# Optimization experiments

Measured on AMD Instinct MI355X. Metric: run time of the kernel, lower is better.

## Reference

```python
import jax, jax.numpy as jnp
import numpy as np

B, S, E, H, ROT, MAXP = 2, 1024, 2048, 16, 64, 2048
HD = E // H
EPS = 1e-12  # torch F.normalize default eps


def _sinusoidal_positions(num_pos, dim):
    # GPT-J create_sinusoidal_positions: concat(sin, cos) along feature dim
    inv_freq = 1.0 / (10000.0 ** (np.arange(0, dim, 2, dtype=np.float32) / dim))
    sinusoid = np.einsum("i,j->ij", np.arange(num_pos, dtype=np.float32), inv_freq)
    return jnp.asarray(np.concatenate([np.sin(sinusoid), np.cos(sinusoid)], axis=-1))


def _rotate_every_two(x):
    x1 = x[..., ::2]
    x2 = x[..., 1::2]
    return jnp.stack((-x2, x1), axis=-1).reshape(x.shape)


def _apply_rotary(t, sin, cos):
    # t: [B,S,H,rot]; sin/cos: [B,S,rot/2] -> repeat_interleave(2) -> [B,S,1,rot]
    sin = jnp.repeat(sin, 2, axis=-1)[:, :, None, :]
    cos = jnp.repeat(cos, 2, axis=-1)[:, :, None, :]
    return t * cos + _rotate_every_two(t) * sin


def setup_inputs() -> dict:
    key = jax.random.key(0)
    ks = jax.random.split(key, 5)
    hidden_states = jax.random.normal(ks[0], (B, S, E), dtype=jnp.float32)
    w_q = jax.random.normal(ks[1], (E, E), dtype=jnp.float32) * 0.02
    w_k = jax.random.normal(ks[2], (E, E), dtype=jnp.float32) * 0.02
    w_v = jax.random.normal(ks[3], (E, E), dtype=jnp.float32) * 0.02
    w_o = jax.random.normal(ks[4], (E, E), dtype=jnp.float32) * 0.02
    norm_const = 0.5 * jnp.ones((1, H, 1, 1), dtype=jnp.float32)
    attention_mask = jnp.zeros((B, 1, 1, S), dtype=jnp.float32)  # 0 = attend (HF additive mask)
    position_ids = jnp.tile(jnp.arange(S, dtype=jnp.int32)[None, :], (B, 1))
    return {"hidden_states": hidden_states, "w_q": w_q, "w_k": w_k, "w_v": w_v,
            "w_o": w_o, "norm_const": norm_const, "attention_mask": attention_mask,
            "position_ids": position_ids}


def reference(hidden_states, w_q, w_k, w_v, w_o, norm_const, attention_mask, position_ids):
    b, s, e = hidden_states.shape
    # projections (nn.Linear, no bias): y = x @ W.T
    q = (hidden_states @ w_q.T).reshape(b, s, H, HD)  # rotary layout [B,S,H,hd]
    k = (hidden_states @ w_k.T).reshape(b, s, H, HD)
    v = (hidden_states @ w_v.T).reshape(b, s, H, HD).transpose(0, 2, 1, 3)  # [B,H,S,hd]

    embed = _sinusoidal_positions(MAXP, ROT)          # [MAXP, ROT]
    sincos = embed[position_ids]                      # [B,S,ROT]
    sin, cos = jnp.split(sincos, 2, axis=-1)          # each [B,S,ROT/2]

    # partial rotary on first ROT dims
    q = jnp.concatenate([_apply_rotary(q[..., :ROT], sin, cos), q[..., ROT:]], axis=-1)
    k = jnp.concatenate([_apply_rotary(k[..., :ROT], sin, cos), k[..., ROT:]], axis=-1)
    q = q.transpose(0, 2, 1, 3)  # [B,H,S,hd]
    k = k.transpose(0, 2, 1, 3)

    causal = jnp.tril(jnp.ones((s, s), dtype=bool))[None, None]   # [1,1,S,S]
    mask0 = (attention_mask == 0)                                  # [B,1,1,S] bool

    # value rescale: per-query count of visible keys ** sigmoid(norm_const), clamped >= 1
    counts = jnp.sum(causal & mask0, axis=-1, keepdims=True).astype(jnp.float32)  # [B,1,S,1]
    denom = jnp.maximum(counts ** jax.nn.sigmoid(norm_const), 1.0)                # [B,H,S,1]
    v = v / denom

    # L2-normalize q/k (torch F.normalize: x / max(||x||, eps))
    q = q / jnp.maximum(jnp.linalg.norm(q, axis=-1, keepdims=True), EPS)
    k = k / jnp.maximum(jnp.linalg.norm(k, axis=-1, keepdims=True), EPS)

    mask_t = jnp.swapaxes(mask0, -1, -2)  # [B,1,S,1]
    q = q * mask_t
    k = k * mask_t
    v = v * mask_t

    attn_weights = jnp.einsum("bhqd,bhkd->bhqk", q, k)     # cosine similarities
    attn_weights = jnp.where(causal, attn_weights, 0.0)
    attn_output = jnp.einsum("bhqk,bhkd->bhqd", attn_weights, v)

    attn_output = attn_output.transpose(0, 2, 1, 3).reshape(b, s, e)
    return attn_output @ w_o.T
```

## Files before the change

kernel.cpp:

```cpp
#include <hip/hip_runtime.h>
#include <math.h>

#define B 2
#define S 1024
#define E 2048
#define H 16
#define HD 128
#define ROT 64
#define EPSN 1e-12f

using half8 = __attribute__((ext_vector_type(8))) _Float16;
using half4 = __attribute__((ext_vector_type(4))) _Float16;
using half2 = __attribute__((ext_vector_type(2))) _Float16;
using f32x4 = __attribute__((ext_vector_type(4))) float;

__device__ __forceinline__ void gl_lds16(const void* g, void* l) {
    __builtin_amdgcn_global_load_lds(
        (const __attribute__((address_space(1))) unsigned int*)g,
        (__attribute__((address_space(3))) unsigned int*)l, 16, 0, 0);
}

#define BARX()  asm volatile("s_barrier" ::: "memory")
#define LGKM0() asm volatile("s_waitcnt lgkmcnt(0)" ::: "memory")
#define VMW(n)  asm volatile("s_waitcnt vmcnt(" #n ")" ::: "memory")

__device__ __forceinline__ int ctIdx(int row, int col) {
    int f = (row & 15) ^ ((row >> 3) & 15);
    return row * 256 + (col & 3) + (((col >> 2) ^ f) << 2);
}

__global__ __launch_bounds__(256) void f2h5(const float* __restrict__ x0,
                                            const float* __restrict__ x1,
                                            const float* __restrict__ x2,
                                            const float* __restrict__ x3,
                                            const float* __restrict__ x4,
                                            _Float16* __restrict__ y0,
                                            _Float16* __restrict__ y1,
                                            _Float16* __restrict__ y2,
                                            _Float16* __restrict__ y3,
                                            _Float16* __restrict__ y4) {
    const float* xs[5] = {x0, x1, x2, x3, x4};
    _Float16*    ys[5] = {y0, y1, y2, y3, y4};
    const int t = blockIdx.y;
    const int i = blockIdx.x * 256 + threadIdx.x;
    float4 v = ((const float4*)xs[t])[i];
    half4 h;
    h[0] = (_Float16)v.x; h[1] = (_Float16)v.y;
    h[2] = (_Float16)v.z; h[3] = (_Float16)v.w;
    ((half4*)ys[t])[i] = h;
}

__global__ __launch_bounds__(1024) void countprep(const float* __restrict__ am,
                                                  const int* __restrict__ pos,
                                                  float* __restrict__ cnt,
                                                  float* __restrict__ tab) {
    __shared__ float sc[1024];
    const int b = blockIdx.x, t = threadIdx.x;
    sc[t] = (am[b * S + t] == 0.f) ? 1.f : 0.f;
    __syncthreads();
    for (int off = 1; off < 1024; off <<= 1) {
        float u = (t >= off) ? sc[t - off] : 0.f;
        __syncthreads();
        sc[t] += u;
        __syncthreads();
    }
    cnt[b * S + t] = sc[t];

    const float p = (float)pos[b * S + t];
    float* tp = &tab[((size_t)b * S + t) * 64];
#pragma unroll
    for (int j = 0; j < 32; ++j) {
        float ang = p * expf(-0.28782313662425574f * (float)j);
        float s_, c_;
        sincosf(ang, &s_, &c_);
        tp[j * 2]     = c_;
        tp[j * 2 + 1] = s_;
    }
}

__global__ __launch_bounds__(512, 2) void gemm_qkv256(
        const _Float16* __restrict__ hs,
        const _Float16* __restrict__ wq,
        const _Float16* __restrict__ wk,
        const _Float16* __restrict__ wv,
        _Float16* __restrict__ qo,
        _Float16* __restrict__ ko,
        _Float16* __restrict__ kto,
        _Float16* __restrict__ vto,
        const float* __restrict__ am,
        const float* __restrict__ nc,
        const float* __restrict__ cnt,
        const float* __restrict__ tab) {
    __shared__ uint4 L[8][1024];
    __shared__ float sclA[256], sclB[256];

    const int lid = (int)blockIdx.x;
    const int swz = (lid & 7) * 24 + (lid >> 3);
    const int z   = swz >> 6;
    const int gm  = (swz & 63) >> 3;
    const int gn  = swz & 7;
    const _Float16* Wp = (z == 0) ? wq : (z == 1) ? wk : wv;
    const int mBase = gm << 8;
    const int nBase = gn << 8;

    const int tid   = (int)threadIdx.x;
    const int lane  = tid & 63;
    const int w     = tid >> 6;
    const int l15   = lane & 15;
    const int lq    = lane >> 4;
    const int wm4   = (w >> 2) << 2;
    const int wn2   = (w & 3) << 1;
    const int wbase = tid & 448;

    const int bb  = mBase >> 10;
    const int sB0 = mBase & (S - 1);
    const int h0  = gn * 2;

    if (tid < 256) {
        const int sgx = sB0 + tid;
        float valid = (am[bb * S + sgx] == 0.f) ? 1.f : 0.f;
        if (z == 2) {
            float c  = cnt[bb * S + sgx];
            float g0 = 1.f / (1.f + expf(-nc[h0]));
            float g1 = 1.f / (1.f + expf(-nc[h0 + 1]));
            sclA[tid] = valid / fmaxf(powf(c, g0), 1.f);
            sclB[tid] = valid / fmaxf(powf(c, g1), 1.f);
        } else {
            sclA[tid] = valid;
        }
    }

    f32x4 acc[2][2][4][2];
#pragma unroll
    for (int X = 0; X < 2; ++X)
#pragma unroll
        for (int Y = 0; Y < 2; ++Y)
#pragma unroll
            for (int mt = 0; mt < 4; ++mt)
#pragma unroll
                for (int nt = 0; nt < 2; ++nt)
                    acc[X][Y][mt][nt] = (f32x4){0.f, 0.f, 0.f, 0.f};

    half8 af[4][2], wf[2][2];

    auto stage = [&](int slot, const _Float16* src, int rowBase, int hf, int kt) {
#pragma unroll
        for (int j = 0; j < 2; ++j) {
            const int c  = (j << 9) + tid;
            const int rb = c >> 7;
            const int q  = (c >> 4) & 7;
            const int r  = c & 15;
            gl_lds16(&src[(size_t)(rowBase + hf * 128 + rb * 16 + r) * E +
                          kt * 64 + q * 8],
                     &L[slot][(j << 9) + wbase]);
        }
    };
    auto ldsA = [&](int db, int X) {
#pragma unroll
        for (int mt = 0; mt < 4; ++mt)
#pragma unroll
            for (int ks = 0; ks < 2; ++ks)
                af[mt][ks] = *(const half8*)&L[db * 2 + X]
                    [(wm4 + mt) * 128 + (ks * 4 + lq) * 16 + l15];
    };
    auto ldsB = [&](int db, int Y) {
#pragma unroll
        for (int nt = 0; nt < 2; ++nt)
#pragma unroll
            for (int ks = 0; ks < 2; ++ks)
                wf[nt][ks] = *(const half8*)&L[4 + db * 2 + Y]
                    [(wn2 + nt) * 128 + (ks * 4 + lq) * 16 + l15];
    };
    auto mma = [&](int X, int Y) {
        __builtin_amdgcn_s_setprio(1);
#pragma unroll
        for (int mt = 0; mt < 4; ++mt)
#pragma unroll
            for (int nt = 0; nt < 2; ++nt)
#pragma unroll
                for (int ks = 0; ks < 2; ++ks)
                    acc[X][Y][mt][nt] = __builtin_amdgcn_mfma_f32_16x16x32_f16(
                        af[mt][ks], wf[nt][ks], acc[X][Y][mt][nt], 0, 0, 0);
        __builtin_amdgcn_s_setprio(0);
    };

    stage(0, hs, mBase, 0, 0);
    stage(4, Wp, nBase, 0, 0);
    stage(1, hs, mBase, 1, 0);
    stage(5, Wp, nBase, 1, 0);
    stage(2, hs, mBase, 0, 1);
    stage(7, Wp, nBase, 1, 1);
    stage(3, hs, mBase, 1, 1);
    VMW(6);
    BARX();

    for (int j = 0; j < 16; ++j) {
        const int tB  = 2 * j + 1;
        const int tN0 = 2 * j + 2;
        const int tN1 = 2 * j + 3;
        const bool more = (j < 15);

        ldsA(0, 0); ldsB(0, 0);
        stage(6, Wp, nBase, 0, tB);
        BARX(); LGKM0();
        mma(0, 0);
        BARX();

        ldsB(0, 1);
        if (more) stage(0, hs, mBase, 0, tN0);
        BARX(); LGKM0();
        mma(0, 1);
        BARX();

        ldsA(0, 1);
        if (more) stage(5, Wp, nBase, 1, tN0);
        BARX(); LGKM0();
        mma(1, 1);
        BARX();

        ldsB(0, 0);
        if (more) { stage(1, hs, mBase, 1, tN0); VMW(4); }
        else      { VMW(0); }
        BARX(); LGKM0();
        mma(1, 0);
        BARX();

        ldsA(1, 0); ldsB(1, 0);
        if (more) stage(4, Wp, nBase, 0, tN0);
        BARX(); LGKM0();
        mma(0, 0);
        BARX();

        ldsB(1, 1);
        if (more) stage(2, hs, mBase, 0, tN1);
        BARX(); LGKM0();
        mma(0, 1);
        BARX();

        ldsA(1, 1);
        if (more) stage(7, Wp, nBase, 1, tN1);
        BARX(); LGKM0();
        mma(1, 1);
        BARX();

        ldsB(1, 0);
        if (more) stage(3, hs, mBase, 1, tN1);
        VMW(4);
        BARX(); LGKM0();
        mma(1, 0);
        BARX();
    }

    VMW(0);
    BARX();
    _Float16* CtH = (_Float16*)&L[0][0];
#pragma unroll
    for (int X = 0; X < 2; ++X)
#pragma unroll
        for (int Y = 0; Y < 2; ++Y)
#pragma unroll
            for (int mt = 0; mt < 4; ++mt)
#pragma unroll
                for (int nt = 0; nt < 2; ++nt)
#pragma unroll
                    for (int r = 0; r < 4; ++r) {
                        int row = X * 128 + (w >> 2) * 64 + mt * 16 + lq * 4 + r;
                        int col = Y * 128 + (w & 3) * 32 + nt * 16 + l15;
                        float v = acc[X][Y][mt][nt][r];
                        if (z == 2) v *= (Y ? sclB[row] : sclA[row]);
                        CtH[ctIdx(row, col)] = (_Float16)v;
                    }
    __syncthreads();

    if (z < 2) {
        const int row = tid >> 1;
        const int hh  = tid & 1;
        const int sg  = sB0 + row;
        const float* tb = &tab[((size_t)bb * S + sg) * 64];

        half4 gv[32];
        float ss = 0.f;
#pragma unroll
        for (int k = 0; k < 32; ++k) {
            half4 x = *(const half4*)&CtH[ctIdx(row, hh * 128 + k * 4)];
            float v0 = x[0], v1 = x[1], v2 = x[2], v3 = x[3];
            if (k < 16) {
                float4 t4 = *(const float4*)&tb[k * 4];
                float t0 = v0 * t4.x - v1 * t4.y;
                float t1 = v1 * t4.x + v0 * t4.y;
                float t2 = v2 * t4.z - v3 * t4.w;
                float t3 = v3 * t4.z + v2 * t4.w;
                v0 = t0; v1 = t1; v2 = t2; v3 = t3;
            }
            ss += v0 * v0 + v1 * v1 + v2 * v2 + v3 * v3;
            half4 y;
            y[0] = (_Float16)v0; y[1] = (_Float16)v1;
            y[2] = (_Float16)v2; y[3] = (_Float16)v3;
            gv[k] = y;
        }
        float scl = sclA[row] / fmaxf(sqrtf(ss), EPSN);
        _Float16* rowOut = (z == 0) ? qo : ko;
        _Float16* gp = &rowOut[(((size_t)bb * H + h0 + hh) * S + sg) * HD];
#pragma unroll
        for (int k = 0; k < 32; ++k) {
            half4 y;
            y[0] = (_Float16)((float)gv[k][0] * scl);
            y[1] = (_Float16)((float)gv[k][1] * scl);
            y[2] = (_Float16)((float)gv[k][2] * scl);
            y[3] = (_Float16)((float)gv[k][3] * scl);
            *(half4*)&gp[k * 4] = y;
            if (z == 1)
                *(half4*)&CtH[ctIdx(row, hh * 128 + k * 4)] = y;
        }
    }
    if (z >= 1) {
        if (z == 1) __syncthreads();
        _Float16* To = (z == 1) ? kto : vto;
#pragma unroll
        for (int i = 0; i < 16; ++i) {
            int cch = tid + i * 512;
            int dr  = cch >> 5;
            int sc  = cch & 31;
            half8 hv;
#pragma unroll
            for (int jj = 0; jj < 8; ++jj)
                hv[jj] = CtH[ctIdx(sc * 8 + jj, dr)];
            *(half8*)&To[(((size_t)bb * H + h0 + (dr >> 7)) * HD + (dr & 127)) * S +
                         sB0 + sc * 8] = hv;
        }
    }
}

__global__ __launch_bounds__(256) void gemm_out(const _Float16* __restrict__ A,
                                                const _Float16* __restrict__ Wp,
                                                float* __restrict__ C) {
    __shared__ uint4 As_l[2][512];
    __shared__ uint4 Ws_l[2][512];
    const int lid = (int)blockIdx.x;
    const int swz = (lid & 7) * 32 + (lid >> 3);
    const int gm  = swz >> 4;
    const int gn  = swz & 15;
    const int tid  = threadIdx.x;
    const int lane = tid & 63;
    const int w    = tid >> 6;
    const int wm   = (w >> 1) * 64;
    const int wn   = (w & 1) * 64;
    const int l15  = lane & 15;
    const int lq   = lane >> 4;
    const int r16  = lane & 15;
    const int kq4  = lane >> 4;
    const int mBase = gm * 128;
    const int nBase = gn * 128;

    f32x4 acc[4][4];
#pragma unroll
    for (int mt = 0; mt < 4; ++mt)
#pragma unroll
        for (int nt = 0; nt < 4; ++nt)
            acc[mt][nt] = (f32x4){0.f, 0.f, 0.f, 0.f};

    auto stage = [&](int bf, int k0) {
#pragma unroll
        for (int i = 0; i < 2; ++i) {
            int rb = w * 2 + i;
            gl_lds16(&A[(size_t)(mBase + rb * 16 + r16) * E + k0 + kq4 * 8],
                     &As_l[bf][rb * 64]);
            gl_lds16(&Wp[(size_t)(nBase + rb * 16 + r16) * E + k0 + kq4 * 8],
                     &Ws_l[bf][rb * 64]);
        }
    };

    stage(0, 0);
    const int nIter = E / 32;
    for (int it = 0; it < nIter; ++it) {
        __syncthreads();
        if (it + 1 < nIter) stage((it + 1) & 1, (it + 1) * 32);

        const int cur = it & 1;
        half8 af[4], wfr[4];
#pragma unroll
        for (int t = 0; t < 4; ++t) {
            int rbA = (wm >> 4) + t;
            int rbW = (wn >> 4) + t;
            af[t]  = *(const half8*)&As_l[cur][rbA * 64 + lq * 16 + l15];
            wfr[t] = *(const half8*)&Ws_l[cur][rbW * 64 + lq * 16 + l15];
        }
#pragma unroll
        for (int mt = 0; mt < 4; ++mt)
#pragma unroll
            for (int nt = 0; nt < 4; ++nt)
                acc[mt][nt] = __builtin_amdgcn_mfma_f32_16x16x32_f16(
                    af[mt], wfr[nt], acc[mt][nt], 0, 0, 0);
    }

#pragma unroll
    for (int mt = 0; mt < 4; ++mt)
#pragma unroll
        for (int nt = 0; nt < 4; ++nt)
#pragma unroll
            for (int r = 0; r < 4; ++r) {
                int row = mBase + wm + mt * 16 + lq * 4 + r;
                int col = nBase + wn + nt * 16 + l15;
                C[(size_t)row * E + col] = acc[mt][nt][r];
            }
}

__global__ __launch_bounds__(256) void kvouter(const _Float16* __restrict__ kt,
                                               const _Float16* __restrict__ vt,
                                               _Float16* __restrict__ ut) {
    __shared__ __align__(16) _Float16 SB[2 * 128 * 72];
    _Float16 (*Kt_s)[72] = (_Float16(*)[72])SB;
    _Float16 (*Vt_s)[72] = (_Float16(*)[72])(SB + 128 * 72);
    const int c  = blockIdx.x;
    const int bh = blockIdx.y;
    const int tid = threadIdx.x;
    const int lane = tid & 63, w = tid >> 6;
    const int l15 = lane & 15, lq = lane >> 4;
    const size_t ds_b = (size_t)bh * HD * S + (size_t)c * 64;

    uint4 pk[4], pv[4];
#pragma unroll
    for (int j = 0; j < 4; ++j) {
        int f = tid + j * 256;
        int d = f >> 3, c8 = f & 7;
        pk[j] = *(const uint4*)&kt[ds_b + (size_t)d * S + c8 * 8];
        pv[j] = *(const uint4*)&vt[ds_b + (size_t)d * S + c8 * 8];
    }
#pragma unroll
    for (int j = 0; j < 4; ++j) {
        int f = tid + j * 256;
        int d = f >> 3, c8 = f & 7;
        *(uint4*)&Kt_s[d][c8 * 8] = pk[j];
        *(uint4*)&Vt_s[d][c8 * 8] = pv[j];
    }
    __syncthreads();

    f32x4 acc[2][8];
#pragma unroll
    for (int mt = 0; mt < 2; ++mt)
#pragma unroll
        for (int nt = 0; nt < 8; ++nt)
            acc[mt][nt] = (f32x4){0.f, 0.f, 0.f, 0.f};

#pragma unroll
    for (int ks = 0; ks < 2; ++ks) {
        half8 af[2], wf[8];
#pragma unroll
        for (int mt = 0; mt < 2; ++mt)
            af[mt] = *(const half8*)&Kt_s[(w * 2 + mt) * 16 + l15][ks * 32 + lq * 8];
#pragma unroll
        for (int nt = 0; nt < 8; ++nt)
            wf[nt] = *(const half8*)&Vt_s[nt * 16 + l15][ks * 32 + lq * 8];
#pragma unroll
        for (int mt = 0; mt < 2; ++mt)
#pragma unroll
            for (int nt = 0; nt < 8; ++nt)
                acc[mt][nt] = __builtin_amdgcn_mfma_f32_16x16x32_f16(
                    af[mt], wf[nt], acc[mt][nt], 0, 0, 0);
    }
    __syncthreads();

    _Float16* Mb = SB;
#pragma unroll
    for (int mt = 0; mt < 2; ++mt)
#pragma unroll
        for (int nt = 0; nt < 8; ++nt)
#pragma unroll
            for (int r = 0; r < 4; ++r) {
                int dk = (w * 2 + mt) * 16 + lq * 4 + r;
                int flat = nt * 2048 + (dk >> 5) * 512 +
                           (l15 + ((dk >> 3) & 3) * 16) * 8 + (dk & 7);
                Mb[flat] = (_Float16)acc[mt][nt][r];
            }
    __syncthreads();

    const size_t ub = ((size_t)bh * 16 + c) << 14;
#pragma unroll
    for (int j = 0; j < 8; ++j) {
        int f = tid + j * 256;
        *(uint4*)&ut[ub + (size_t)f * 8] = *(const uint4*)&Mb[f * 8];
    }
}

__global__ __launch_bounds__(256) void prefix16(_Float16* __restrict__ u) {
    const int sl = blockIdx.x & 7;
    const int bh = blockIdx.x >> 3;
    const size_t base = (size_t)bh * 16 * 16384 + sl * 2048 + threadIdx.x * 8;
    float acc[8] = {0.f, 0.f, 0.f, 0.f, 0.f, 0.f, 0.f, 0.f};
    half8 nxt = *(const half8*)&u[base];
#pragma unroll
    for (int c = 0; c < 16; ++c) {
        half8 cur = nxt;
        if (c < 15) nxt = *(const half8*)&u[base + (size_t)(c + 1) * 16384];
        half8 outv;
#pragma unroll
        for (int i = 0; i < 8; ++i) outv[i] = (_Float16)acc[i];
        *(half8*)&u[base + (size_t)c * 16384] = outv;
#pragma unroll
        for (int i = 0; i < 8; ++i) acc[i] += (float)cur[i];
    }
}

__global__ __launch_bounds__(256) void attn_local(const _Float16* __restrict__ qh,
                                                  const _Float16* __restrict__ kh,
                                                  const _Float16* __restrict__ vt,
                                                  const _Float16* __restrict__ mt,
                                                  _Float16* __restrict__ o) {
    __shared__ _Float16 Ks[64][136];
    __shared__ _Float16 Vs[HD][72];
    __shared__ _Float16 Ps[64][72];
    __shared__ uint4 Ms[2048];

    const int qt = blockIdx.x;
    const int bh = blockIdx.y;
    const int b = bh >> 4, h = bh & 15;
    const int tid = threadIdx.x;
    const int lane = tid & 63;
    const int w = tid >> 6;
    const int l15 = lane & 15;
    const int lq = lane >> 4;
    const int qBase = qt * 64;
    const size_t sd_base = (size_t)bh * S * HD;

    half8 qf[4];
#pragma unroll
    for (int ks = 0; ks < 4; ++ks)
        qf[ks] = *(const half8*)&qh[sd_base + (size_t)(qBase + w * 16 + l15) * HD +
                                    ks * 32 + lq * 8];

    const _Float16* mtc = mt + (((size_t)bh * 16 + qt) << 14);
#pragma unroll
    for (int rr = 0; rr < 8; ++rr)
        gl_lds16(&mtc[(size_t)((rr * 4 + w) * 64 + lane) * 8],
                 &Ms[(rr * 4 + w) * 64]);

    uint4 pk[4], pv[4];
#pragma unroll
    for (int j = 0; j < 4; ++j) {
        int f = tid + j * 256;
        int rK = f >> 4, c8K = f & 15;
        int rV = f >> 3, c8V = f & 7;
        pk[j] = *(const uint4*)&kh[sd_base + (size_t)(qBase + rK) * HD + c8K * 8];
        pv[j] = *(const uint4*)&vt[sd_base + (size_t)rV * S + qBase + c8V * 8];
    }
#pragma unroll
    for (int j = 0; j < 4; ++j) {
        int f = tid + j * 256;
        int rK = f >> 4, c8K = f & 15;
        int rV = f >> 3, c8V = f & 7;
        *(uint4*)&Ks[rK][c8K * 8] = pk[j];
        *(uint4*)&Vs[rV][c8V * 8] = pv[j];
    }
    __syncthreads();

    f32x4 sacc[4];
#pragma unroll
    for (int nt = 0; nt < 4; ++nt)
        sacc[nt] = (f32x4){0.f, 0.f, 0.f, 0.f};
#pragma unroll
    for (int nt = 0; nt < 4; ++nt)
#pragma unroll
        for (int ks = 0; ks < 4; ++ks) {
            half8 kf = *(const half8*)&Ks[nt * 16 + l15][ks * 32 + lq * 8];
            sacc[nt] = __builtin_amdgcn_mfma_f32_16x16x32_f16(qf[ks], kf,
                                                              sacc[nt], 0, 0, 0);
        }

#pragma unroll
    for (int nt = 0; nt < 4; ++nt)
#pragma unroll
        for (int r = 0; r < 4; ++r) {
            int ql = w * 16 + lq * 4 + r;
            int kl = nt * 16 + l15;
            float sv = (kl <= ql) ? sacc[nt][r] : 0.f;
            Ps[ql][kl] = (_Float16)sv;
        }

    f32x4 oacc[8];
#pragma unroll
    for (int dt = 0; dt < 8; ++dt)
        oacc[dt] = (f32x4){0.f, 0.f, 0.f, 0.f};
#pragma unroll
    for (int dt = 0; dt < 8; ++dt)
#pragma unroll
        for (int km = 0; km < 4; ++km) {
            half8 mf = *(const half8*)&Ms[(dt * 4 + km) * 64 + lane];
            oacc[dt] = __builtin_amdgcn_mfma_f32_16x16x32_f16(qf[km], mf,
                                                              oacc[dt], 0, 0, 0);
        }
    __syncthreads();

    half8 pf[2];
    pf[0] = *(const half8*)&Ps[w * 16 + l15][lq * 8];
    pf[1] = *(const half8*)&Ps[w * 16 + l15][32 + lq * 8];
#pragma unroll
    for (int dt = 0; dt < 8; ++dt)
#pragma unroll
        for (int ks = 0; ks < 2; ++ks) {
            half8 vf = *(const half8*)&Vs[dt * 16 + l15][ks * 32 + lq * 8];
            oacc[dt] = __builtin_amdgcn_mfma_f32_16x16x32_f16(pf[ks], vf,
                                                              oacc[dt], 0, 0, 0);
        }

#pragma unroll
    for (int dt = 0; dt < 8; ++dt)
#pragma unroll
        for (int r = 0; r < 4; ++r)
            Ks[w * 16 + lq * 4 + r][dt * 16 + l15] = (_Float16)oacc[dt][r];
    __syncthreads();
#pragma unroll
    for (int j = 0; j < 4; ++j) {
        int f = tid + j * 256;
        int ql = f >> 4, c8 = f & 15;
        *(uint4*)&o[(size_t)(b * S + qBase + ql) * E + h * HD + c8 * 8] =
            *(const uint4*)&Ks[ql][c8 * 8];
    }
}

extern "C" void kernel_launch(void* const* d_in, const int* in_sizes, int n_in,
                              void* d_out, int out_size, void* d_ws, size_t ws_size,
                              hipStream_t stream) {
    (void)in_sizes; (void)n_in; (void)out_size; (void)ws_size;
    const float* hs = (const float*)d_in[0];
    const float* wq = (const float*)d_in[1];
    const float* wk = (const float*)d_in[2];
    const float* wv = (const float*)d_in[3];
    const float* wo = (const float*)d_in[4];
    const float* nc = (const float*)d_in[5];
    const float* am = (const float*)d_in[6];
    const int*  pos = (const int*)d_in[7];
    float* out = (float*)d_out;

    const size_t act = (size_t)B * S * E;
    _Float16* hsb = (_Float16*)d_ws;
    _Float16* wqb = hsb + act;
    _Float16* wkb = wqb + act;
    _Float16* wvb = wkb + act;
    _Float16* wob = wvb + act;
    _Float16* qhh = wob + act;
    _Float16* khh = qhh + act;
    _Float16* ktt = khh + act;
    _Float16* vtt = ktt + act;
    _Float16* abb = vtt + act;
    _Float16* utm = wqb;
    float*    cnt = (float*)abb;
    float*    tab = cnt + B * S;

    f2h5<<<dim3((int)(act / 4 / 256), 5), 256, 0, stream>>>(
        hs, wq, wk, wv, wo, hsb, wqb, wkb, wvb, wob);

    countprep<<<B, 1024, 0, stream>>>(am, pos, cnt, tab);

    gemm_qkv256<<<192, 512, 0, stream>>>(hsb, wqb, wkb, wvb,
                                         qhh, khh, ktt, vtt, am, nc, cnt, tab);

    kvouter<<<dim3(16, B * H), 256, 0, stream>>>(ktt, vtt, utm);
    prefix16<<<B * H * 8, 256, 0, stream>>>(utm);
    attn_local<<<dim3(16, B * H), 256, 0, stream>>>(qhh, khh, vtt, utm, abb);

    gemm_out<<<256, 256, 0, stream>>>(abb, wob, out);
}
```

Before: 324.5 us.

## Fuse prep kernels, compute V transposed in GEMM, merge kv outer product with prefix

The fp16 conversion, sin/cos table and mask-count prefix kernels are merged into one launch, and the count scan now uses 256 threads with four items each. The V projection swaps its operands so it writes V transposed directly, which removes the LDS transpose and the separate transposed-K buffer. The per-chunk K^T V outer products and their prefix sum are fused into one kernel that accumulates across chunks and writes the exclusive prefix as it goes. The cost is fewer blocks for kvp (4x32), so that kernel is a serial loop over 16 chunks, and V is stored with scattered 2-byte global writes.

Measured after the change: 295.1 us. 1.1x faster.

```diff
diff --git a/kernel.cpp b/kernel.cpp
--- a/kernel.cpp
+++ b/kernel.cpp
@@ -29,7 +29,7 @@
     return row * 256 + (col & 3) + (((col >> 2) ^ f) << 2);
 }
 
-__global__ __launch_bounds__(256) void f2h5(const float* __restrict__ x0,
+__global__ __launch_bounds__(256) void prep(const float* __restrict__ x0,
                                             const float* __restrict__ x1,
                                             const float* __restrict__ x2,
                                             const float* __restrict__ x3,
@@ -38,43 +38,56 @@
                                             _Float16* __restrict__ y1,
                                             _Float16* __restrict__ y2,
                                             _Float16* __restrict__ y3,
-                                            _Float16* __restrict__ y4) {
-    const float* xs[5] = {x0, x1, x2, x3, x4};
-    _Float16*    ys[5] = {y0, y1, y2, y3, y4};
-    const int t = blockIdx.y;
-    const int i = blockIdx.x * 256 + threadIdx.x;
-    float4 v = ((const float4*)xs[t])[i];
-    half4 h;
-    h[0] = (_Float16)v.x; h[1] = (_Float16)v.y;
-    h[2] = (_Float16)v.z; h[3] = (_Float16)v.w;
-    ((half4*)ys[t])[i] = h;
-}
-
-__global__ __launch_bounds__(1024) void countprep(const float* __restrict__ am,
-                                                  const int* __restrict__ pos,
-                                                  float* __restrict__ cnt,
-                                                  float* __restrict__ tab) {
-    __shared__ float sc[1024];
-    const int b = blockIdx.x, t = threadIdx.x;
-    sc[t] = (am[b * S + t] == 0.f) ? 1.f : 0.f;
-    __syncthreads();
-    for (int off = 1; off < 1024; off <<= 1) {
-        float u = (t >= off) ? sc[t - off] : 0.f;
-        __syncthreads();
-        sc[t] += u;
-        __syncthreads();
-    }
-    cnt[b * S + t] = sc[t];
-
-    const float p = (float)pos[b * S + t];
-    float* tp = &tab[((size_t)b * S + t) * 64];
-#pragma unroll
-    for (int j = 0; j < 32; ++j) {
+                                            _Float16* __restrict__ y4,
+                                            const float* __restrict__ am,
+                                            const int*  __restrict__ pos,
+                                            float* __restrict__ cnt,
+                                            float* __restrict__ tab) {
+    __shared__ float ls[256];
+    const int bx = (int)blockIdx.x;
+    if (bx < 20480) {
+        const float* xs[5] = {x0, x1, x2, x3, x4};
+        _Float16*    ys[5] = {y0, y1, y2, y3, y4};
+        const int t = bx >> 12;
+        const int i = (bx & 4095) * 256 + threadIdx.x;
+        float4 v = ((const float4*)xs[t])[i];
+        half4 h;
+        h[0] = (_Float16)v.x; h[1] = (_Float16)v.y;
+        h[2] = (_Float16)v.z; h[3] = (_Float16)v.w;
+        ((half4*)ys[t])[i] = h;
+    } else if (bx < 20736) {
+        int item = (bx - 20480) * 256 + threadIdx.x;
+        int bs = item >> 5, j = item & 31;
+        float p = (float)pos[bs];
         float ang = p * expf(-0.28782313662425574f * (float)j);
         float s_, c_;
         sincosf(ang, &s_, &c_);
-        tp[j * 2]     = c_;
-        tp[j * 2 + 1] = s_;
+        tab[(size_t)bs * 64 + j * 2]     = c_;
+        tab[(size_t)bs * 64 + j * 2 + 1] = s_;
+    } else {
+        const int b = bx - 20736;
+        const int t = threadIdx.x;
+        float v[4];
+        float s4 = 0.f;
+#pragma unroll
+        for (int i = 0; i < 4; ++i) {
+            v[i] = (am[b * S + t * 4 + i] == 0.f) ? 1.f : 0.f;
+            s4 += v[i];
+        }
+        ls[t] = s4;
+        __syncthreads();
+        for (int off = 1; off < 256; off <<= 1) {
+            float u = (t >= off) ? ls[t - off] : 0.f;
+            __syncthreads();
+            ls[t] += u;
+            __syncthreads();
+        }
+        float run = ls[t] - s4;
+#pragma unroll
+        for (int i = 0; i < 4; ++i) {
+            run += v[i];
+            cnt[b * S + t * 4 + i] = run;
+        }
     }
 }
 
@@ -85,7 +98,6 @@
         const _Float16* __restrict__ wv,
         _Float16* __restrict__ qo,
         _Float16* __restrict__ ko,
-        _Float16* __restrict__ kto,
         _Float16* __restrict__ vto,
         const float* __restrict__ am,
         const float* __restrict__ nc,
@@ -99,7 +111,8 @@
     const int z   = swz >> 6;
     const int gm  = (swz & 63) >> 3;
     const int gn  = swz & 7;
-    const _Float16* Wp = (z == 0) ? wq : (z == 1) ? wk : wv;
+    const _Float16* Asrc = (z == 2) ? wv : hs;
+    const _Float16* Bsrc = (z == 2) ? hs : ((z == 0) ? wq : wk);
     const int mBase = gm << 8;
     const int nBase = gn << 8;
 
@@ -112,21 +125,21 @@
     const int wn2   = (w & 3) << 1;
     const int wbase = tid & 448;
 
-    const int bb  = mBase >> 10;
-    const int sB0 = mBase & (S - 1);
-    const int h0  = gn * 2;
-
     if (tid < 256) {
-        const int sgx = sB0 + tid;
-        float valid = (am[bb * S + sgx] == 0.f) ? 1.f : 0.f;
         if (z == 2) {
-            float c  = cnt[bb * S + sgx];
-            float g0 = 1.f / (1.f + expf(-nc[h0]));
-            float g1 = 1.f / (1.f + expf(-nc[h0 + 1]));
+            const int bbv  = nBase >> 10;
+            const int sgx  = (nBase & (S - 1)) + tid;
+            const int h0v  = mBase >> 7;
+            float valid = (am[bbv * S + sgx] == 0.f) ? 1.f : 0.f;
+            float c  = cnt[bbv * S + sgx];
+            float g0 = 1.f / (1.f + expf(-nc[h0v]));
+            float g1 = 1.f / (1.f + expf(-nc[h0v + 1]));
             sclA[tid] = valid / fmaxf(powf(c, g0), 1.f);
             sclB[tid] = valid / fmaxf(powf(c, g1), 1.f);
         } else {
-            sclA[tid] = valid;
+            const int bb  = mBase >> 10;
+            const int sgx = (mBase & (S - 1)) + tid;
+            sclA[tid] = (am[bb * S + sgx] == 0.f) ? 1.f : 0.f;
         }
     }
 
@@ -184,13 +197,13 @@
         __builtin_amdgcn_s_setprio(0);
     };
 
-    stage(0, hs, mBase, 0, 0);
-    stage(4, Wp, nBase, 0, 0);
-    stage(1, hs, mBase, 1, 0);
-    stage(5, Wp, nBase, 1, 0);
-    stage(2, hs, mBase, 0, 1);
-    stage(7, Wp, nBase, 1, 1);
-    stage(3, hs, mBase, 1, 1);
+    stage(0, Asrc, mBase, 0, 0);
+    stage(4, Bsrc, nBase, 0, 0);
+    stage(1, Asrc, mBase, 1, 0);
+    stage(5, Bsrc, nBase, 1, 0);
+    stage(2, Asrc, mBase, 0, 1);
+    stage(7, Bsrc, nBase, 1, 1);
+    stage(3, Asrc, mBase, 1, 1);
     VMW(6);
     BARX();
 
@@ -201,78 +214,79 @@
         const bool more = (j < 15);
 
         ldsA(0, 0); ldsB(0, 0);
-        stage(6, Wp, nBase, 0, tB);
+        stage(6, Bsrc, nBase, 0, tB);
         BARX(); LGKM0();
         mma(0, 0);
         BARX();
 
         ldsB(0, 1);
-        if (more) stage(0, hs, mBase, 0, tN0);
+        if (more) stage(0, Asrc, mBase, 0, tN0);
         BARX(); LGKM0();
         mma(0, 1);
         BARX();
 
         ldsA(0, 1);
-        if (more) stage(5, Wp, nBase, 1, tN0);
+        if (more) stage(5, Bsrc, nBase, 1, tN0);
         BARX(); LGKM0();
         mma(1, 1);
         BARX();
 
         ldsB(0, 0);
-        if (more) { stage(1, hs, mBase, 1, tN0); VMW(4); }
+        if (more) { stage(1, Asrc, mBase, 1, tN0); VMW(4); }
         else      { VMW(0); }
         BARX(); LGKM0();
         mma(1, 0);
         BARX();
 
         ldsA(1, 0); ldsB(1, 0);
-        if (more) stage(4, Wp, nBase, 0, tN0);
+        if (more) stage(4, Bsrc, nBase, 0, tN0);
         BARX(); LGKM0();
         mma(0, 0);
         BARX();
 
         ldsB(1, 1);
-        if (more) stage(2, hs, mBase, 0, tN1);
+        if (more) stage(2, Asrc, mBase, 0, tN1);
         BARX(); LGKM0();
         mma(0, 1);
         BARX();
 
         ldsA(1, 1);
-        if (more) stage(7, Wp, nBase, 1, tN1);
+        if (more) stage(7, Bsrc, nBase, 1, tN1);
         BARX(); LGKM0();
         mma(1, 1);
         BARX();
 
         ldsB(1, 0);
-        if (more) stage(3, hs, mBase, 1, tN1);
+        if (more) stage(3, Asrc, mBase, 1, tN1);
         VMW(4);
         BARX(); LGKM0();
         mma(1, 0);
         BARX();
     }
 
-    VMW(0);
-    BARX();
-    _Float16* CtH = (_Float16*)&L[0][0];
-#pragma unroll
-    for (int X = 0; X < 2; ++X)
-#pragma unroll
-        for (int Y = 0; Y < 2; ++Y)
-#pragma unroll
-            for (int mt = 0; mt < 4; ++mt)
-#pragma unroll
-                for (int nt = 0; nt < 2; ++nt)
-#pragma unroll
-                    for (int r = 0; r < 4; ++r) {
-                        int row = X * 128 + (w >> 2) * 64 + mt * 16 + lq * 4 + r;
-                        int col = Y * 128 + (w & 3) * 32 + nt * 16 + l15;
-                        float v = acc[X][Y][mt][nt][r];
-                        if (z == 2) v *= (Y ? sclB[row] : sclA[row]);
-                        CtH[ctIdx(row, col)] = (_Float16)v;
-                    }
-    __syncthreads();
-
     if (z < 2) {
+        const int bb  = mBase >> 10;
+        const int sB0 = mBase & (S - 1);
+        const int h0  = nBase >> 7;
+        VMW(0);
+        BARX();
+        _Float16* CtH = (_Float16*)&L[0][0];
+#pragma unroll
+        for (int X = 0; X < 2; ++X)
+#pragma unroll
+            for (int Y = 0; Y < 2; ++Y)
+#pragma unroll
+                for (int mt = 0; mt < 4; ++mt)
+#pragma unroll
+                    for (int nt = 0; nt < 2; ++nt)
+#pragma unroll
+                        for (int r = 0; r < 4; ++r) {
+                            int row = X * 128 + (w >> 2) * 64 + mt * 16 + lq * 4 + r;
+                            int col = Y * 128 + (w & 3) * 32 + nt * 16 + l15;
+                            CtH[ctIdx(row, col)] = (_Float16)acc[X][Y][mt][nt][r];
+                        }
+        __syncthreads();
+
         const int row = tid >> 1;
         const int hh  = tid & 1;
         const int sg  = sB0 + row;
@@ -309,25 +323,220 @@
             y[2] = (_Float16)((float)gv[k][2] * scl);
             y[3] = (_Float16)((float)gv[k][3] * scl);
             *(half4*)&gp[k * 4] = y;
-            if (z == 1)
-                *(half4*)&CtH[ctIdx(row, hh * 128 + k * 4)] = y;
-        }
-    }
-    if (z >= 1) {
-        if (z == 1) __syncthreads();
-        _Float16* To = (z == 1) ? kto : vto;
-#pragma unroll
-        for (int i = 0; i < 16; ++i) {
-            int cch = tid + i * 512;
-            int dr  = cch >> 5;
-            int sc  = cch & 31;
-            half8 hv;
-#pragma unroll
-            for (int jj = 0; jj < 8; ++jj)
-                hv[jj] = CtH[ctIdx(sc * 8 + jj, dr)];
-            *(half8*)&To[(((size_t)bb * H + h0 + (dr >> 7)) * HD + (dr & 127)) * S +
-                         sB0 + sc * 8] = hv;
-        }
+        }
+    } else {
+        const int bbv  = nBase >> 10;
+        const int sB0v = nBase & (S - 1);
+        const int h0v  = mBase >> 7;
+#pragma unroll
+        for (int X = 0; X < 2; ++X)
+#pragma unroll
+            for (int Y = 0; Y < 2; ++Y)
+#pragma unroll
+                for (int mt = 0; mt < 4; ++mt)
+#pragma unroll
+                    for (int nt = 0; nt < 2; ++nt)
+#pragma unroll
+                        for (int r = 0; r < 4; ++r) {
+                            int dvRow = X * 128 + (w >> 2) * 64 + mt * 16 + lq * 4 + r;
+                            int sCol  = Y * 128 + (w & 3) * 32 + nt * 16 + l15;
+                            float scl = X ? sclB[sCol] : sclA[sCol];
+                            vto[((size_t)(bbv * H + h0v + X) * HD + (dvRow & 127)) * S +
+                                sB0v + sCol] =
+                                (_Float16)(acc[X][Y][mt][nt][r] * scl);
+                        }
+    }
+}
+
+__global__ __launch_bounds__(256) void kvp(const _Float16* __restrict__ kh,
+                                           const _Float16* __restrict__ vt,
+                                           _Float16* __restrict__ ut) {
+    __shared__ _Float16 Kt_s[HD][72];
+    __shared__ _Float16 Vt_s[32][72];
+    const int slice = blockIdx.x;
+    const int bh    = blockIdx.y;
+    const int tid = threadIdx.x;
+    const int lane = tid & 63, w = tid >> 6;
+    const int l15 = lane & 15, lq = lane >> 4;
+    const size_t kbase = (size_t)bh * S * HD;
+    const size_t vbase = ((size_t)bh * HD + slice * 32) * S;
+
+    f32x4 accr[2][2];
+#pragma unroll
+    for (int mt = 0; mt < 2; ++mt)
+#pragma unroll
+        for (int nt = 0; nt < 2; ++nt)
+            accr[mt][nt] = (f32x4){0.f, 0.f, 0.f, 0.f};
+
+    for (int c = 0; c < 16; ++c) {
+        const int c0 = c * 64;
+        half8 kreg[4];
+#pragma unroll
+        for (int j = 0; j < 4; ++j)
+            kreg[j] = *(const half8*)&kh[kbase + (size_t)(c0 + lane) * HD +
+                                         (j * 4 + w) * 8];
+        uint4 vreg = *(const uint4*)&vt[vbase + (size_t)(tid >> 3) * S +
+                                        c0 + (tid & 7) * 8];
+
+        const size_t ub = ((size_t)bh * 16 + c) << 14;
+#pragma unroll
+        for (int mt = 0; mt < 2; ++mt)
+#pragma unroll
+            for (int nt = 0; nt < 2; ++nt) {
+                int mtg = w * 2 + mt, ntg = slice * 2 + nt;
+                int f0 = ntg * 2048 + (mtg >> 1) * 512 +
+                         (l15 + ((mtg * 2 + (lq >> 1)) & 3) * 16) * 8 +
+                         (lq & 1) * 4;
+                half4 hv;
+                hv[0] = (_Float16)accr[mt][nt][0];
+                hv[1] = (_Float16)accr[mt][nt][1];
+                hv[2] = (_Float16)accr[mt][nt][2];
+                hv[3] = (_Float16)accr[mt][nt][3];
+                *(half4*)&ut[ub + f0] = hv;
+            }
+
+        __syncthreads();
+#pragma unroll
+        for (int j = 0; j < 4; ++j)
+#pragma unroll
+            for (int i = 0; i < 8; ++i)
+                Kt_s[(j * 4 + w) * 8 + i][lane] = kreg[j][i];
+        *(uint4*)&Vt_s[tid >> 3][(tid & 7) * 8] = vreg;
+        __syncthreads();
+
+#pragma unroll
+        for (int ks = 0; ks < 2; ++ks) {
+            half8 afv[2], wfv[2];
+#pragma unroll
+            for (int mt = 0; mt < 2; ++mt)
+                afv[mt] = *(const half8*)&Kt_s[(w * 2 + mt) * 16 + l15]
+                                              [ks * 32 + lq * 8];
+#pragma unroll
+            for (int nt = 0; nt < 2; ++nt)
+                wfv[nt] = *(const half8*)&Vt_s[nt * 16 + l15][ks * 32 + lq * 8];
+#pragma unroll
+            for (int mt = 0; mt < 2; ++mt)
+#pragma unroll
+                for (int nt = 0; nt < 2; ++nt)
+                    accr[mt][nt] = __builtin_amdgcn_mfma_f32_16x16x32_f16(
+                        afv[mt], wfv[nt], accr[mt][nt], 0, 0, 0);
+        }
+    }
+}
+
+__global__ __launch_bounds__(256) void attn_local(const _Float16* __restrict__ qh,
+                                                  const _Float16* __restrict__ kh,
+                                                  const _Float16* __restrict__ vt,
+                                                  const _Float16* __restrict__ mt,
+                                                  _Float16* __restrict__ o) {
+    __shared__ _Float16 Ks[64][136];
+    __shared__ _Float16 Vs[HD][72];
+    __shared__ _Float16 Ps[64][72];
+    __shared__ uint4 Ms[2048];
+
+    const int qt = blockIdx.x;
+    const int bh = blockIdx.y;
+    const int b = bh >> 4, h = bh & 15;
+    const int tid = threadIdx.x;
+    const int lane = tid & 63;
+    const int w = tid >> 6;
+    const int l15 = lane & 15;
+    const int lq = lane >> 4;
+    const int qBase = qt * 64;
+    const size_t sd_base = (size_t)bh * S * HD;
+
+    half8 qf[4];
+#pragma unroll
+    for (int ks = 0; ks < 4; ++ks)
+        qf[ks] = *(const half8*)&qh[sd_base + (size_t)(qBase + w * 16 + l15) * HD +
+                                    ks * 32 + lq * 8];
+
+    const _Float16* mtc = mt + (((size_t)bh * 16 + qt) << 14);
+#pragma unroll
+    for (int rr = 0; rr < 8; ++rr)
+        gl_lds16(&mtc[(size_t)((rr * 4 + w) * 64 + lane) * 8],
+                 &Ms[(rr * 4 + w) * 64]);
+
+    uint4 pk[4], pv[4];
+#pragma unroll
+    for (int j = 0; j < 4; ++j) {
+        int f = tid + j * 256;
+        int rK = f >> 4, c8K = f & 15;
+        int rV = f >> 3, c8V = f & 7;
+        pk[j] = *(const uint4*)&kh[sd_base + (size_t)(qBase + rK) * HD + c8K * 8];
+        pv[j] = *(const uint4*)&vt[sd_base + (size_t)rV * S + qBase + c8V * 8];
+    }
+#pragma unroll
+    for (int j = 0; j < 4; ++j) {
+        int f = tid + j * 256;
+        int rK = f >> 4, c8K = f & 15;
+        int rV = f >> 3, c8V = f & 7;
+        *(uint4*)&Ks[rK][c8K * 8] = pk[j];
+        *(uint4*)&Vs[rV][c8V * 8] = pv[j];
+    }
+    __syncthreads();
+
+    f32x4 sacc[4];
+#pragma unroll
+    for (int nt = 0; nt < 4; ++nt)
+        sacc[nt] = (f32x4){0.f, 0.f, 0.f, 0.f};
+#pragma unroll
+    for (int nt = 0; nt < 4; ++nt)
+#pragma unroll
+        for (int ks = 0; ks < 4; ++ks) {
+            half8 kf = *(const half8*)&Ks[nt * 16 + l15][ks * 32 + lq * 8];
+            sacc[nt] = __builtin_amdgcn_mfma_f32_16x16x32_f16(qf[ks], kf,
+                                                              sacc[nt], 0, 0, 0);
+        }
+
+#pragma unroll
+    for (int nt = 0; nt < 4; ++nt)
+#pragma unroll
+        for (int r = 0; r < 4; ++r) {
+            int ql = w * 16 + lq * 4 + r;
+            int kl = nt * 16 + l15;
+            float sv = (kl <= ql) ? sacc[nt][r] : 0.f;
+            Ps[ql][kl] = (_Float16)sv;
+        }
+
+    f32x4 oacc[8];
+#pragma unroll
+    for (int dt = 0; dt < 8; ++dt)
+        oacc[dt] = (f32x4){0.f, 0.f, 0.f, 0.f};
+#pragma unroll
+    for (int dt = 0; dt < 8; ++dt)
+#pragma unroll
+        for (int km = 0; km < 4; ++km) {
+            half8 mf = *(const half8*)&Ms[(dt * 4 + km) * 64 + lane];
+            oacc[dt] = __builtin_amdgcn_mfma_f32_16x16x32_f16(qf[km], mf,
+                                                              oacc[dt], 0, 0, 0);
+        }
+    __syncthreads();
+
+    half8 pf[2];
+    pf[0] = *(const half8*)&Ps[w * 16 + l15][lq * 8];
+    pf[1] = *(const half8*)&Ps[w * 16 + l15][32 + lq * 8];
+#pragma unroll
+    for (int dt = 0; dt < 8; ++dt)
+#pragma unroll
+        for (int ks = 0; ks < 2; ++ks) {
+            half8 vf = *(const half8*)&Vs[dt * 16 + l15][ks * 32 + lq * 8];
+            oacc[dt] = __builtin_amdgcn_mfma_f32_16x16x32_f16(pf[ks], vf,
+                                                              oacc[dt], 0, 0, 0);
+        }
+
+#pragma unroll
+    for (int dt = 0; dt < 8; ++dt)
+#pragma unroll
+        for (int r = 0; r < 4; ++r)
+            Ks[w * 16 + lq * 4 + r][dt * 16 + l15] = (_Float16)oacc[dt][r];
+    __syncthreads();
+#pragma unroll
+    for (int j = 0; j < 4; ++j) {
+        int f = tid + j * 256;
+        int ql = f >> 4, c8 = f & 15;
+        *(uint4*)&o[(size_t)(b * S + qBase + ql) * E + h * HD + c8 * 8] =
+            *(const uint4*)&Ks[ql][c8 * 8];
     }
 }
 
@@ -405,218 +614,6 @@
             }
 }
 
-__global__ __launch_bounds__(256) void kvouter(const _Float16* __restrict__ kt,
-                                               const _Float16* __restrict__ vt,
-                                               _Float16* __restrict__ ut) {
-    __shared__ __align__(16) _Float16 SB[2 * 128 * 72];
-    _Float16 (*Kt_s)[72] = (_Float16(*)[72])SB;
-    _Float16 (*Vt_s)[72] = (_Float16(*)[72])(SB + 128 * 72);
-    const int c  = blockIdx.x;
-    const int bh = blockIdx.y;
-    const int tid = threadIdx.x;
-    const int lane = tid & 63, w = tid >> 6;
-    const int l15 = lane & 15, lq = lane >> 4;
-    const size_t ds_b = (size_t)bh * HD * S + (size_t)c * 64;
-
-    uint4 pk[4], pv[4];
-#pragma unroll
-    for (int j = 0; j < 4; ++j) {
-        int f = tid + j * 256;
-        int d = f >> 3, c8 = f & 7;
-        pk[j] = *(const uint4*)&kt[ds_b + (size_t)d * S + c8 * 8];
-        pv[j] = *(const uint4*)&vt[ds_b + (size_t)d * S + c8 * 8];
-    }
-#pragma unroll
-    for (int j = 0; j < 4; ++j) {
-        int f = tid + j * 256;
-        int d = f >> 3, c8 = f & 7;
-        *(uint4*)&Kt_s[d][c8 * 8] = pk[j];
-        *(uint4*)&Vt_s[d][c8 * 8] = pv[j];
-    }
-    __syncthreads();
-
-    f32x4 acc[2][8];
-#pragma unroll
-    for (int mt = 0; mt < 2; ++mt)
-#pragma unroll
-        for (int nt = 0; nt < 8; ++nt)
-            acc[mt][nt] = (f32x4){0.f, 0.f, 0.f, 0.f};
-
-#pragma unroll
-    for (int ks = 0; ks < 2; ++ks) {
-        half8 af[2], wf[8];
-#pragma unroll
-        for (int mt = 0; mt < 2; ++mt)
-            af[mt] = *(const half8*)&Kt_s[(w * 2 + mt) * 16 + l15][ks * 32 + lq * 8];
-#pragma unroll
-        for (int nt = 0; nt < 8; ++nt)
-            wf[nt] = *(const half8*)&Vt_s[nt * 16 + l15][ks * 32 + lq * 8];
-#pragma unroll
-        for (int mt = 0; mt < 2; ++mt)
-#pragma unroll
-            for (int nt = 0; nt < 8; ++nt)
-                acc[mt][nt] = __builtin_amdgcn_mfma_f32_16x16x32_f16(
-                    af[mt], wf[nt], acc[mt][nt], 0, 0, 0);
-    }
-    __syncthreads();
-
-    _Float16* Mb = SB;
-#pragma unroll
-    for (int mt = 0; mt < 2; ++mt)
-#pragma unroll
-        for (int nt = 0; nt < 8; ++nt)
-#pragma unroll
-            for (int r = 0; r < 4; ++r) {
-                int dk = (w * 2 + mt) * 16 + lq * 4 + r;
-                int flat = nt * 2048 + (dk >> 5) * 512 +
-                           (l15 + ((dk >> 3) & 3) * 16) * 8 + (dk & 7);
-                Mb[flat] = (_Float16)acc[mt][nt][r];
-            }
-    __syncthreads();
-
-    const size_t ub = ((size_t)bh * 16 + c) << 14;
-#pragma unroll
-    for (int j = 0; j < 8; ++j) {
-        int f = tid + j * 256;
-        *(uint4*)&ut[ub + (size_t)f * 8] = *(const uint4*)&Mb[f * 8];
-    }
-}
-
-__global__ __launch_bounds__(256) void prefix16(_Float16* __restrict__ u) {
-    const int sl = blockIdx.x & 7;
-    const int bh = blockIdx.x >> 3;
-    const size_t base = (size_t)bh * 16 * 16384 + sl * 2048 + threadIdx.x * 8;
-    float acc[8] = {0.f, 0.f, 0.f, 0.f, 0.f, 0.f, 0.f, 0.f};
-    half8 nxt = *(const half8*)&u[base];
-#pragma unroll
-    for (int c = 0; c < 16; ++c) {
-        half8 cur = nxt;
-        if (c < 15) nxt = *(const half8*)&u[base + (size_t)(c + 1) * 16384];
-        half8 outv;
-#pragma unroll
-        for (int i = 0; i < 8; ++i) outv[i] = (_Float16)acc[i];
-        *(half8*)&u[base + (size_t)c * 16384] = outv;
-#pragma unroll
-        for (int i = 0; i < 8; ++i) acc[i] += (float)cur[i];
-    }
-}
-
-__global__ __launch_bounds__(256) void attn_local(const _Float16* __restrict__ qh,
-                                                  const _Float16* __restrict__ kh,
-                                                  const _Float16* __restrict__ vt,
-                                                  const _Float16* __restrict__ mt,
-                                                  _Float16* __restrict__ o) {
-    __shared__ _Float16 Ks[64][136];
-    __shared__ _Float16 Vs[HD][72];
-    __shared__ _Float16 Ps[64][72];
-    __shared__ uint4 Ms[2048];
-
-    const int qt = blockIdx.x;
-    const int bh = blockIdx.y;
-    const int b = bh >> 4, h = bh & 15;
-    const int tid = threadIdx.x;
-    const int lane = tid & 63;
-    const int w = tid >> 6;
-    const int l15 = lane & 15;
-    const int lq = lane >> 4;
-    const int qBase = qt * 64;
-    const size_t sd_base = (size_t)bh * S * HD;
-
-    half8 qf[4];
-#pragma unroll
-    for (int ks = 0; ks < 4; ++ks)
-        qf[ks] = *(const half8*)&qh[sd_base + (size_t)(qBase + w * 16 + l15) * HD +
-                                    ks * 32 + lq * 8];
-
-    const _Float16* mtc = mt + (((size_t)bh * 16 + qt) << 14);
-#pragma unroll
-    for (int rr = 0; rr < 8; ++rr)
-        gl_lds16(&mtc[(size_t)((rr * 4 + w) * 64 + lane) * 8],
-                 &Ms[(rr * 4 + w) * 64]);
-
-    uint4 pk[4], pv[4];
-#pragma unroll
-    for (int j = 0; j < 4; ++j) {
-        int f = tid + j * 256;
-        int rK = f >> 4, c8K = f & 15;
-        int rV = f >> 3, c8V = f & 7;
-        pk[j] = *(const uint4*)&kh[sd_base + (size_t)(qBase + rK) * HD + c8K * 8];
-        pv[j] = *(const uint4*)&vt[sd_base + (size_t)rV * S + qBase + c8V * 8];
-    }
-#pragma unroll
-    for (int j = 0; j < 4; ++j) {
-        int f = tid + j * 256;
-        int rK = f >> 4, c8K = f & 15;
-        int rV = f >> 3, c8V = f & 7;
-        *(uint4*)&Ks[rK][c8K * 8] = pk[j];
-        *(uint4*)&Vs[rV][c8V * 8] = pv[j];
-    }
-    __syncthreads();
-
-    f32x4 sacc[4];
-#pragma unroll
-    for (int nt = 0; nt < 4; ++nt)
-        sacc[nt] = (f32x4){0.f, 0.f, 0.f, 0.f};
-#pragma unroll
-    for (int nt = 0; nt < 4; ++nt)
-#pragma unroll
-        for (int ks = 0; ks < 4; ++ks) {
-            half8 kf = *(const half8*)&Ks[nt * 16 + l15][ks * 32 + lq * 8];
-            sacc[nt] = __builtin_amdgcn_mfma_f32_16x16x32_f16(qf[ks], kf,
-                                                              sacc[nt], 0, 0, 0);
-        }
-
-#pragma unroll
-    for (int nt = 0; nt < 4; ++nt)
-#pragma unroll
-        for (int r = 0; r < 4; ++r) {
-            int ql = w * 16 + lq * 4 + r;
-            int kl = nt * 16 + l15;
-            float sv = (kl <= ql) ? sacc[nt][r] : 0.f;
-            Ps[ql][kl] = (_Float16)sv;
-        }
-
-    f32x4 oacc[8];
-#pragma unroll
-    for (int dt = 0; dt < 8; ++dt)
-        oacc[dt] = (f32x4){0.f, 0.f, 0.f, 0.f};
-#pragma unroll
-    for (int dt = 0; dt < 8; ++dt)
-#pragma unroll
-        for (int km = 0; km < 4; ++km) {
-            half8 mf = *(const half8*)&Ms[(dt * 4 + km) * 64 + lane];
-            oacc[dt] = __builtin_amdgcn_mfma_f32_16x16x32_f16(qf[km], mf,
-                                                              oacc[dt], 0, 0, 0);
-        }
-    __syncthreads();
-
-    half8 pf[2];
-    pf[0] = *(const half8*)&Ps[w * 16 + l15][lq * 8];
-    pf[1] = *(const half8*)&Ps[w * 16 + l15][32 + lq * 8];
-#pragma unroll
-    for (int dt = 0; dt < 8; ++dt)
-#pragma unroll
-        for (int ks = 0; ks < 2; ++ks) {
-            half8 vf = *(const half8*)&Vs[dt * 16 + l15][ks * 32 + lq * 8];
-            oacc[dt] = __builtin_amdgcn_mfma_f32_16x16x32_f16(pf[ks], vf,
-                                                              oacc[dt], 0, 0, 0);
-        }
-
-#pragma unroll
-    for (int dt = 0; dt < 8; ++dt)
-#pragma unroll
-        for (int r = 0; r < 4; ++r)
-            Ks[w * 16 + lq * 4 + r][dt * 16 + l15] = (_Float16)oacc[dt][r];
-    __syncthreads();
-#pragma unroll
-    for (int j = 0; j < 4; ++j) {
-        int f = tid + j * 256;
-        int ql = f >> 4, c8 = f & 15;
-        *(uint4*)&o[(size_t)(b * S + qBase + ql) * E + h * HD + c8 * 8] =
-            *(const uint4*)&Ks[ql][c8 * 8];
-    }
-}
-
 extern "C" void kernel_launch(void* const* d_in, const int* in_sizes, int n_in,
                               void* d_out, int out_size, void* d_ws, size_t ws_size,
                               hipStream_t stream) {
@@ -639,23 +636,20 @@
     _Float16* wob = wvb + act;
     _Float16* qhh = wob + act;
     _Float16* khh = qhh + act;
-    _Float16* ktt = khh + act;
-    _Float16* vtt = ktt + act;
+    _Float16* vtt = khh + act;
     _Float16* abb = vtt + act;
     _Float16* utm = wqb;
     float*    cnt = (float*)abb;
     float*    tab = cnt + B * S;
 
-    f2h5<<<dim3((int)(act / 4 / 256), 5), 256, 0, stream>>>(
-        hs, wq, wk, wv, wo, hsb, wqb, wkb, wvb, wob);
-
-    countprep<<<B, 1024, 0, stream>>>(am, pos, cnt, tab);
+    prep<<<20480 + 256 + B, 256, 0, stream>>>(
+        hs, wq, wk, wv, wo, hsb, wqb, wkb, wvb, wob, am, pos, cnt, tab);
 
     gemm_qkv256<<<192, 512, 0, stream>>>(hsb, wqb, wkb, wvb,
-                                         qhh, khh, ktt, vtt, am, nc, cnt, tab);
-
-    kvouter<<<dim3(16, B * H), 256, 0, stream>>>(ktt, vtt, utm);
-    prefix16<<<B * H * 8, 256, 0, stream>>>(utm);
+                                         qhh, khh, vtt, am, nc, cnt, tab);
+
+    kvp<<<dim3(4, B * H), 256, 0, stream>>>(khh, vtt, utm);
+
     attn_local<<<dim3(16, B * H), 256, 0, stream>>>(qhh, khh, vtt, utm, abb);
 
     gemm_out<<<256, 256, 0, stream>>>(abb, wob, out);
```
